# Performance work log

Hardware: AMD Instinct MI355X
Metric: run time of the kernel (lower is better)

The kernel has to match this reference:

```python
import jax, jax.numpy as jnp
import numpy as np

HIDDEN = 4096
NUM_HEADS = 32
HEAD_DIM = HIDDEN // NUM_HEADS  # 128, used only as softmax scale
CACHE_LEN = 100
BATCH = 8192


def setup_inputs() -> dict:
    key = jax.random.key(0)
    ks = jax.random.split(key, 7)
    return {
        "x": jax.random.normal(ks[0], (BATCH, HIDDEN), dtype=jnp.float32),
        "q_w": jax.random.normal(ks[1], (HIDDEN, HIDDEN), dtype=jnp.float32) * (1.0 / np.sqrt(HIDDEN)),
        "q_b": jax.random.normal(ks[2], (HIDDEN,), dtype=jnp.float32) * 0.01,
        "k_cache": jax.random.normal(ks[3], (CACHE_LEN, HIDDEN), dtype=jnp.float32),
        "v_cache": jax.random.normal(ks[4], (CACHE_LEN, HIDDEN), dtype=jnp.float32),
        "out_w": jax.random.normal(ks[5], (HIDDEN, HIDDEN), dtype=jnp.float32) * (1.0 / np.sqrt(HIDDEN)),
        "out_b": jax.random.normal(ks[6], (HIDDEN,), dtype=jnp.float32) * 0.01,
    }


def reference(x, q_w, q_b, k_cache, v_cache, out_w, out_b):
    # q_proj: torch Linear -> x @ W^T + b
    q = x @ q_w.T + q_b                                   # [N, H]
    # concat one zero row onto each cache (kv_len = CACHE_LEN + 1)
    k = jnp.concatenate([k_cache, jnp.zeros_like(k_cache[:1])], axis=0)  # [L+1, H]
    v = jnp.concatenate([v_cache, jnp.zeros_like(v_cache[:1])], axis=0)  # [L+1, H]
    scale = 1.0 / np.sqrt(HEAD_DIM).astype(np.float32)
    scores = (q @ k.T) * scale                            # [N, L+1]
    weights = jax.nn.softmax(scores, axis=-1)
    attn = weights @ v                                    # [N, H]
    return attn @ out_w.T + out_b                         # [N, H]
```

## Files before the change

kernel.cpp:

```cpp
#include <hip/hip_runtime.h>
#include <cstdio>

typedef __attribute__((ext_vector_type(8))) short short8;
typedef __attribute__((ext_vector_type(4))) float f32x4;


__device__ __forceinline__ unsigned short bf16r(float f) {
  union { float f; unsigned int u; } x; x.f = f;
  unsigned int r = x.u + 0x7fffu + ((x.u >> 16) & 1u);
  return (unsigned short)(r >> 16);
}

__device__ __forceinline__ float bf16f(unsigned short h) {
  union { unsigned int u; float f; } x; x.u = ((unsigned int)h) << 16;
  return x.f;
}

__device__ __forceinline__ void gload_lds16(const void* g, void* l) {
  __builtin_amdgcn_global_load_lds((const __attribute__((address_space(1))) void*)g,
                                   (__attribute__((address_space(3))) void*)l,
                                   16, 0, 0);
}

__device__ __forceinline__ short8 pack_bf16(float4 f0, float4 f1) {
  short8 h;
  h[0] = (short)bf16r(f0.x); h[1] = (short)bf16r(f0.y);
  h[2] = (short)bf16r(f0.z); h[3] = (short)bf16r(f0.w);
  h[4] = (short)bf16r(f1.x); h[5] = (short)bf16r(f1.y);
  h[6] = (short)bf16r(f1.z); h[7] = (short)bf16r(f1.w);
  return h;
}


__global__ void build_pad128(const float* __restrict__ src, unsigned short* __restrict__ dst) {
  int idx = blockIdx.x * blockDim.x + threadIdx.x;
  if (idx >= 128 * 4096) return;
  int row = idx >> 12;
  float v = (row < 100) ? src[idx] : 0.f;
  dst[idx] = bf16r(v);
}

__global__ void kq_bias(const float* __restrict__ kc, const float* __restrict__ qb,
                        float* __restrict__ sbias) {
  int l = blockIdx.x;
  int lane = threadIdx.x;
  float s = 0.f;
  if (l < 100) {
    for (int i = lane * 4; i < 4096; i += 256) {
      float4 k = *reinterpret_cast<const float4*>(kc + (size_t)l * 4096 + i);
      float4 q = *reinterpret_cast<const float4*>(qb + i);
      s += k.x * q.x + k.y * q.y + k.z * q.z + k.w * q.w;
    }
  }
  #pragma unroll
  for (int off = 1; off < 64; off <<= 1) s += __shfl_xor(s, off);
  if (lane == 0) sbias[l] = s;
}


__global__ __launch_bounds__(256)
void kq_fused(const unsigned short* __restrict__ Kp,
              const float* __restrict__ Qw,
              float* __restrict__ Cpart,
              int H, int jchunk) {
  __shared__ unsigned short Ak[128][32];
  __shared__ float Ts[32][129];

  const int tid = threadIdx.x, wave = tid >> 6, lane = tid & 63;
  const int wm = wave >> 1, wn = wave & 1;
  const int j0 = blockIdx.x * jchunk;
  const int i0 = blockIdx.y * 128;

  const int sr = wave * 16 + (lane >> 2);
  const int sc = (lane & 3) << 3;
  const unsigned short* Kp0 = Kp + (size_t)sr * H + j0 + sc;
  const unsigned short* Kp1 = Kp + (size_t)(64 + sr) * H + j0 + sc;
  unsigned short* AD0 = &Ak[wave * 16][0];
  unsigned short* AD1 = &Ak[64 + wave * 16][0];

  const int tj = tid >> 3;
  const int tc = (tid & 7) * 16;
  const float* Qp = Qw + (size_t)(j0 + tj) * H + i0 + tc;

  const int fr = lane & 15;
  const int kq = lane >> 4;

  f32x4 acc[4][4] = {};

  for (int jj = 0; jj < jchunk; jj += 32) {
    gload_lds16(Kp0 + jj, AD0);
    gload_lds16(Kp1 + jj, AD1);
    {
      const float* q = Qp + (size_t)jj * H;
      float4 v0 = *reinterpret_cast<const float4*>(q);
      float4 v1 = *reinterpret_cast<const float4*>(q + 4);
      float4 v2 = *reinterpret_cast<const float4*>(q + 8);
      float4 v3 = *reinterpret_cast<const float4*>(q + 12);
      Ts[tj][tc + 0]  = v0.x; Ts[tj][tc + 1]  = v0.y; Ts[tj][tc + 2]  = v0.z; Ts[tj][tc + 3]  = v0.w;
      Ts[tj][tc + 4]  = v1.x; Ts[tj][tc + 5]  = v1.y; Ts[tj][tc + 6]  = v1.z; Ts[tj][tc + 7]  = v1.w;
      Ts[tj][tc + 8]  = v2.x; Ts[tj][tc + 9]  = v2.y; Ts[tj][tc + 10] = v2.z; Ts[tj][tc + 11] = v2.w;
      Ts[tj][tc + 12] = v3.x; Ts[tj][tc + 13] = v3.y; Ts[tj][tc + 14] = v3.z; Ts[tj][tc + 15] = v3.w;
    }
    __syncthreads();

    short8 av[4];
    #pragma unroll
    for (int mi = 0; mi < 4; ++mi)
      av[mi] = *reinterpret_cast<const short8*>(&Ak[wm * 64 + mi * 16 + fr][kq * 8]);

    short8 bhi[4], blo[4];
    #pragma unroll
    for (int ni = 0; ni < 4; ++ni) {
      const int ic = wn * 64 + ni * 16 + fr;
      #pragma unroll
      for (int s = 0; s < 8; ++s) {
        float f = Ts[kq * 8 + s][ic];
        unsigned short h = bf16r(f);
        bhi[ni][s] = (short)h;
        blo[ni][s] = (short)bf16r(f - bf16f(h));
      }
    }

    #pragma unroll
    for (int mi = 0; mi < 4; ++mi)
      #pragma unroll
      for (int ni = 0; ni < 4; ++ni) {
        acc[mi][ni] = __builtin_amdgcn_mfma_f32_16x16x32_bf16(av[mi], bhi[ni], acc[mi][ni], 0, 0, 0);
        acc[mi][ni] = __builtin_amdgcn_mfma_f32_16x16x32_bf16(av[mi], blo[ni], acc[mi][ni], 0, 0, 0);
      }
    __syncthreads();
  }

  float* Cp = Cpart + (size_t)blockIdx.x * 128 * H;
  const int orow = (lane >> 4) * 4;
  const int ocol = lane & 15;
  #pragma unroll
  for (int mi = 0; mi < 4; ++mi) {
    #pragma unroll
    for (int ni = 0; ni < 4; ++ni) {
      size_t r0 = (size_t)wm * 64 + mi * 16 + orow;
      size_t c  = (size_t)i0 + wn * 64 + ni * 16 + ocol;
      #pragma unroll
      for (int j = 0; j < 4; ++j)
        Cp[(r0 + j) * (size_t)H + c] = acc[mi][ni][j];
    }
  }
}


template<int NB>
__global__ __launch_bounds__(256, 1)
void gemm_sv(const float* __restrict__ A, const unsigned short* __restrict__ B,
             float* __restrict__ Cpart, int M, int Kstride, int kchunk) {
  constexpr int FOLD = NB / 128;
  __shared__ float          As[2][128][32];
  __shared__ unsigned short Bs[2][NB][32];

  const int tid = threadIdx.x, wave = tid >> 6, lane = tid & 63;
  const int wm = wave >> 1, wn = wave & 1;
  const int ks = blockIdx.x, mblk = blockIdx.y;
  const size_t rowA0 = (size_t)mblk * 128;
  const int k0 = ks * kchunk;
  const int nsteps = kchunk >> 5;

  const int ar = lane >> 3;
  const int as_g = (lane & 7) ^ ar;
  const int br = lane >> 2;
  const int bs_g = (lane & 3) ^ (br & 3);

#define STAGE_SV(kt, BUF) do { \
    const int _kc = k0 + (kt) * 32; \
    _Pragma("unroll") \
    for (int j = 0; j < 4; ++j) \
      gload_lds16(A + (rowA0 + wave * 32 + j * 8 + ar) * (size_t)Kstride + _kc + as_g * 4, \
                  &As[BUF][wave * 32 + j * 8][0]); \
    _Pragma("unroll") \
    for (int j = 0; j < NB / 64; ++j) \
      gload_lds16(B + (size_t)(wave * (NB / 4) + j * 16 + br) * Kstride + _kc + bs_g * 8, \
                  &Bs[BUF][wave * (NB / 4) + j * 16][0]); \
  } while (0)

#define WAIT_STAGE do { \
    if (NB == 256) asm volatile("s_waitcnt vmcnt(8)" ::: "memory"); \
    else           asm volatile("s_waitcnt vmcnt(6)" ::: "memory"); \
  } while (0)

  const int fr = lane & 15, kq = lane >> 4;
  f32x4 acc[4][4] = {};

  STAGE_SV(0, 0);
  STAGE_SV(1, 1);
  WAIT_STAGE;
  asm volatile("" ::: "memory");
  __builtin_amdgcn_s_barrier();
  asm volatile("" ::: "memory");

  for (int k = 0; k < nsteps; ++k) {
    const int c = k & 1;

    short8 av[4], bv[4][FOLD];
    #pragma unroll
    for (int mi = 0; mi < 4; ++mi) {
      const float* rp = &As[c][wm * 64 + mi * 16 + fr][0];
      float4 f0 = *reinterpret_cast<const float4*>(rp + (((2 * kq)     ^ (fr & 7)) * 4));
      float4 f1 = *reinterpret_cast<const float4*>(rp + (((2 * kq + 1) ^ (fr & 7)) * 4));
      av[mi] = pack_bf16(f0, f1);
    }
    #pragma unroll
    for (int ni = 0; ni < 4; ++ni)
      #pragma unroll
      for (int p = 0; p < FOLD; ++p) {
        int rb = p * 128 + wn * 64 + ni * 16 + fr;
        bv[ni][p] = *reinterpret_cast<const short8*>(&Bs[c][rb][0] + ((kq ^ (fr & 3)) * 8));
      }

    asm volatile("s_waitcnt lgkmcnt(0)" ::: "memory");
    __builtin_amdgcn_s_barrier();
    asm volatile("" ::: "memory");

    const int kt2 = (k + 2 < nsteps) ? k + 2 : nsteps - 1;
    STAGE_SV(kt2, c);
    asm volatile("" ::: "memory");

    __builtin_amdgcn_s_setprio(1);
    #pragma unroll
    for (int mi = 0; mi < 4; ++mi)
      #pragma unroll
      for (int ni = 0; ni < 4; ++ni)
        #pragma unroll
        for (int p = 0; p < FOLD; ++p)
          acc[mi][ni] = __builtin_amdgcn_mfma_f32_16x16x32_bf16(av[mi], bv[ni][p], acc[mi][ni], 0, 0, 0);
    __builtin_amdgcn_s_setprio(0);

    WAIT_STAGE;
    asm volatile("" ::: "memory");
    __builtin_amdgcn_s_barrier();
    asm volatile("" ::: "memory");
  }

#undef STAGE_SV
#undef WAIT_STAGE

  float* Cp = Cpart + (size_t)ks * M * 128;
  const int orow = (lane >> 4) * 4;
  const int ocol = lane & 15;
  #pragma unroll
  for (int mi = 0; mi < 4; ++mi) {
    #pragma unroll
    for (int ni = 0; ni < 4; ++ni) {
      size_t r0 = rowA0 + wm * 64 + mi * 16 + orow;
      size_t c  = (size_t)wn * 64 + ni * 16 + ocol;
      #pragma unroll
      for (int j = 0; j < 4; ++j)
        Cp[(r0 + j) * 128 + c] = acc[mi][ni][j];
    }
  }
}


__global__ void kq_reduce(const float* __restrict__ KQpart, unsigned short* __restrict__ KQ2) {
  int idx = blockIdx.x * blockDim.x + threadIdx.x;
  if (idx >= 128 * 4096) return;
  float s = 0.f;
  #pragma unroll
  for (int ks = 0; ks < 8; ++ks) s += KQpart[(size_t)ks * 128 * 4096 + idx];
  unsigned short hi = bf16r(s);
  unsigned short lo = bf16r(s - bf16f(hi));
  int l = idx >> 12, j = idx & 4095;
  KQ2[(size_t)l * 4096 + j]         = hi;
  KQ2[(size_t)(l + 128) * 4096 + j] = lo;
}


__global__ void softmax_fused2(const float* __restrict__ Spart, const float* __restrict__ sbias,
                               unsigned short* __restrict__ W2, int rows) {
  int wave = threadIdx.x >> 6;
  int lane = threadIdx.x & 63;
  int row = blockIdx.x * (blockDim.x >> 6) + wave;
  if (row >= rows) return;
  const float scale = 0.088388347648318447f;
  float sx = 0.f, sy = 0.f;
  #pragma unroll
  for (int ks = 0; ks < 8; ++ks) {
    float2 p = reinterpret_cast<const float2*>(Spart + ((size_t)ks * rows + row) * 128)[lane];
    sx += p.x; sy += p.y;
  }
  float2 bb = reinterpret_cast<const float2*>(sbias)[lane];
  sx += bb.x; sy += bb.y;
  int c0 = lane * 2, c1 = c0 + 1;
  float s0 = (c0 <= 100) ? sx * scale : -1e30f;
  float s1 = (c1 <= 100) ? sy * scale : -1e30f;
  float m = fmaxf(s0, s1);
  #pragma unroll
  for (int off = 1; off < 64; off <<= 1) m = fmaxf(m, __shfl_xor(m, off));
  float e0 = (c0 <= 100) ? __expf(s0 - m) : 0.f;
  float e1 = (c1 <= 100) ? __expf(s1 - m) : 0.f;
  float sum = e0 + e1;
  #pragma unroll
  for (int off = 1; off < 64; off <<= 1) sum += __shfl_xor(sum, off);
  float inv = 1.f / sum;
  ushort2 o;
  o.x = bf16r(e0 * inv);
  o.y = bf16r(e1 * inv);
  reinterpret_cast<ushort2*>(W2 + (size_t)row * 256)[lane] = o;
  reinterpret_cast<ushort2*>(W2 + (size_t)row * 256 + 128)[lane] = o;
}


__global__ void vo_reduce(const float* __restrict__ VOpart, unsigned short* __restrict__ VOT2) {
  int idx = blockIdx.x * blockDim.x + threadIdx.x;
  if (idx >= 4096 * 128) return;
  float s = 0.f;
  #pragma unroll
  for (int ks = 0; ks < 16; ++ks) s += VOpart[(size_t)ks * 4096 * 128 + idx];
  unsigned short hi = bf16r(s);
  unsigned short lo = bf16r(s - bf16f(hi));
  int o = idx >> 7, l = idx & 127;
  VOT2[(size_t)o * 256 + l]       = hi;
  VOT2[(size_t)o * 256 + 128 + l] = lo;
}


__global__ __launch_bounds__(256)
void gemm_final(const unsigned short* __restrict__ A,
                const unsigned short* __restrict__ B,
                const float* __restrict__ bias,
                float* __restrict__ Cout,
                int M, int N, int K) {
  __shared__ unsigned short As[128][40];
  __shared__ unsigned short Bs[128][40];

  const int tid = threadIdx.x, wave = tid >> 6, lane = tid & 63;
  const int wm = wave >> 1, wn = wave & 1;
  const size_t rowA0 = (size_t)blockIdx.y * 128;
  const size_t colB0 = (size_t)blockIdx.x * 128;

  f32x4 acc[4][4] = {};

  const int srow  = tid >> 1;
  const int shalf = (tid & 1) * 16;

  const unsigned short* Ap = A + (rowA0 + srow) * (size_t)K + shalf;
  const unsigned short* Bp = B + (colB0 + srow) * (size_t)K + shalf;

  const int fr = lane & 15;
  const int fk = (lane >> 4) << 3;

  for (int k0 = 0; k0 < K; k0 += 32) {
    short8 a0 = *reinterpret_cast<const short8*>(Ap + k0);
    short8 a1 = *reinterpret_cast<const short8*>(Ap + k0 + 8);
    short8 b0 = *reinterpret_cast<const short8*>(Bp + k0);
    short8 b1 = *reinterpret_cast<const short8*>(Bp + k0 + 8);
    *reinterpret_cast<short8*>(&As[srow][shalf])     = a0;
    *reinterpret_cast<short8*>(&As[srow][shalf + 8]) = a1;
    *reinterpret_cast<short8*>(&Bs[srow][shalf])     = b0;
    *reinterpret_cast<short8*>(&Bs[srow][shalf + 8]) = b1;
    __syncthreads();

    short8 av[4], bv[4];
    #pragma unroll
    for (int mi = 0; mi < 4; ++mi)
      av[mi] = *reinterpret_cast<const short8*>(&As[wm * 64 + mi * 16 + fr][fk]);
    #pragma unroll
    for (int ni = 0; ni < 4; ++ni)
      bv[ni] = *reinterpret_cast<const short8*>(&Bs[wn * 64 + ni * 16 + fr][fk]);
    #pragma unroll
    for (int mi = 0; mi < 4; ++mi)
      #pragma unroll
      for (int ni = 0; ni < 4; ++ni)
        acc[mi][ni] = __builtin_amdgcn_mfma_f32_16x16x32_bf16(av[mi], bv[ni], acc[mi][ni], 0, 0, 0);
    __syncthreads();
  }

  const int orow = (lane >> 4) * 4;
  const int ocol = lane & 15;
  #pragma unroll
  for (int mi = 0; mi < 4; ++mi) {
    #pragma unroll
    for (int ni = 0; ni < 4; ++ni) {
      size_t r0 = rowA0 + wm * 64 + mi * 16 + orow;
      size_t c  = colB0 + wn * 64 + ni * 16 + ocol;
      float bv_ = bias[c];
      #pragma unroll
      for (int j = 0; j < 4; ++j)
        Cout[(r0 + j) * (size_t)N + c] = acc[mi][ni][j] + bv_;
    }
  }
}


extern "C" void kernel_launch(void* const* d_in, const int* in_sizes, int n_in,
                              void* d_out, int out_size, void* d_ws, size_t ws_size,
                              hipStream_t stream) {
  const float* x       = (const float*)d_in[0];
  const float* q_w     = (const float*)d_in[1];
  const float* q_b     = (const float*)d_in[2];
  const float* k_cache = (const float*)d_in[3];
  const float* v_cache = (const float*)d_in[4];
  const float* out_w   = (const float*)d_in[5];
  const float* out_b   = (const float*)d_in[6];
  float* out = (float*)d_out;

  const int M = 8192, H = 4096;

  char* ws = (char*)d_ws;
  size_t off = 0;
  auto alloc = [&](size_t bytes) { void* p = ws + off; off += (bytes + 255) & ~(size_t)255; return p; };
  unsigned short* kpad   = (unsigned short*)alloc((size_t)128 * H * 2);
  unsigned short* vpad   = (unsigned short*)alloc((size_t)128 * H * 2);
  float*          sbias  = (float*)alloc(128 * 4);
  unsigned short* KQ2    = (unsigned short*)alloc((size_t)256 * H * 2);
  unsigned short* W2     = (unsigned short*)alloc((size_t)M * 256 * 2);
  unsigned short* VOT2   = (unsigned short*)alloc((size_t)H * 256 * 2);
  float*          scratch= (float*)alloc((size_t)36 << 20);
  if (ws_size < off) { fprintf(stderr, "ws too small: need %zu have %zu\n", off, ws_size); return; }

  build_pad128<<<2048, 256, 0, stream>>>(k_cache, kpad);
  build_pad128<<<2048, 256, 0, stream>>>(v_cache, vpad);
  kq_bias<<<128, 64, 0, stream>>>(k_cache, q_b, sbias);

  kq_fused<<<dim3(8, 32), 256, 0, stream>>>(kpad, q_w, scratch, H, 512);
  kq_reduce<<<2048, 256, 0, stream>>>(scratch, KQ2);

  gemm_sv<256><<<dim3(8, 64), 256, 0, stream>>>(x, KQ2, scratch, M, H, 512);

  softmax_fused2<<<M / 4, 256, 0, stream>>>(scratch, sbias, W2, M);

  gemm_sv<128><<<dim3(16, 32), 256, 0, stream>>>(out_w, vpad, scratch, H, H, 256);
  vo_reduce<<<2048, 256, 0, stream>>>(scratch, VOT2);

  gemm_final<<<dim3(32, 64), 256, 0, stream>>>(W2, VOT2, out_b, out, M, H, 256);
}
```

Before: 188.4 us.

## Merge independent small kernels into horizontally fused launches to cut launch count

Result: faster. 162.0 us (median of 3 runs) (-14.0%).

```diff
diff --git a/kernel.cpp b/kernel.cpp
--- a/kernel.cpp
+++ b/kernel.cpp
@@ -32,44 +32,49 @@
 }
 
 
-__global__ void build_pad128(const float* __restrict__ src, unsigned short* __restrict__ dst) {
-  int idx = blockIdx.x * blockDim.x + threadIdx.x;
-  if (idx >= 128 * 4096) return;
-  int row = idx >> 12;
-  float v = (row < 100) ? src[idx] : 0.f;
-  dst[idx] = bf16r(v);
-}
-
-__global__ void kq_bias(const float* __restrict__ kc, const float* __restrict__ qb,
-                        float* __restrict__ sbias) {
-  int l = blockIdx.x;
-  int lane = threadIdx.x;
-  float s = 0.f;
-  if (l < 100) {
-    for (int i = lane * 4; i < 4096; i += 256) {
-      float4 k = *reinterpret_cast<const float4*>(kc + (size_t)l * 4096 + i);
-      float4 q = *reinterpret_cast<const float4*>(qb + i);
-      s += k.x * q.x + k.y * q.y + k.z * q.z + k.w * q.w;
-    }
-  }
-  #pragma unroll
-  for (int off = 1; off < 64; off <<= 1) s += __shfl_xor(s, off);
-  if (lane == 0) sbias[l] = s;
-}
-
-
-__global__ __launch_bounds__(256)
-void kq_fused(const unsigned short* __restrict__ Kp,
-              const float* __restrict__ Qw,
-              float* __restrict__ Cpart,
-              int H, int jchunk) {
-  __shared__ unsigned short Ak[128][32];
-  __shared__ float Ts[32][129];
+__global__ void prep(const float* __restrict__ kc, const float* __restrict__ vc,
+                     const float* __restrict__ qb,
+                     unsigned short* __restrict__ kpad, unsigned short* __restrict__ vpad,
+                     float* __restrict__ sbias) {
+  const int b = blockIdx.x, tid = threadIdx.x;
+  if (b < 4096) {
+    const bool isK = b < 2048;
+    const int bb = isK ? b : b - 2048;
+    int idx = bb * 256 + tid;
+    int row = idx >> 12;
+    const float* src = isK ? kc : vc;
+    float v = (row < 100) ? src[idx] : 0.f;
+    (isK ? kpad : vpad)[idx] = bf16r(v);
+  } else {
+    const int wave = tid >> 6, lane = tid & 63;
+    const int l = (b - 4096) * 4 + wave;
+    float s = 0.f;
+    if (l < 100) {
+      for (int i = lane * 4; i < 4096; i += 256) {
+        float4 k = *reinterpret_cast<const float4*>(kc + (size_t)l * 4096 + i);
+        float4 q = *reinterpret_cast<const float4*>(qb + i);
+        s += k.x * q.x + k.y * q.y + k.z * q.z + k.w * q.w;
+      }
+    }
+    #pragma unroll
+    for (int off = 1; off < 64; off <<= 1) s += __shfl_xor(s, off);
+    if (lane == 0) sbias[l] = s;
+  }
+}
+
+
+__device__ __forceinline__ void kq_fused_body(const unsigned short* __restrict__ Kp,
+                                              const float* __restrict__ Qw,
+                                              float* __restrict__ Cpart,
+                                              int H, int jchunk, int js, int itile,
+                                              char* smem) {
+  unsigned short (*Ak)[32] = (unsigned short (*)[32])smem;
+  float (*Ts)[129] = (float (*)[129])(smem + 8192);
 
   const int tid = threadIdx.x, wave = tid >> 6, lane = tid & 63;
   const int wm = wave >> 1, wn = wave & 1;
-  const int j0 = blockIdx.x * jchunk;
-  const int i0 = blockIdx.y * 128;
+  const int j0 = js * jchunk;
+  const int i0 = itile * 128;
 
   const int sr = wave * 16 + (lane >> 2);
   const int sc = (lane & 3) << 3;
@@ -131,7 +136,7 @@
     __syncthreads();
   }
 
-  float* Cp = Cpart + (size_t)blockIdx.x * 128 * H;
+  float* Cp = Cpart + (size_t)js * 128 * H;
   const int orow = (lane >> 4) * 4;
   const int ocol = lane & 15;
   #pragma unroll
@@ -149,16 +154,17 @@
 
 
 template<int NB>
-__global__ __launch_bounds__(256, 1)
-void gemm_sv(const float* __restrict__ A, const unsigned short* __restrict__ B,
-             float* __restrict__ Cpart, int M, int Kstride, int kchunk) {
+__device__ __forceinline__ void gemm_sv_body(const float* __restrict__ A,
+                                             const unsigned short* __restrict__ B,
+                                             float* __restrict__ Cpart,
+                                             int M, int Kstride, int kchunk,
+                                             int ks, int mblk, char* smem) {
   constexpr int FOLD = NB / 128;
-  __shared__ float          As[2][128][32];
-  __shared__ unsigned short Bs[2][NB][32];
+  float (*As)[128][32] = (float (*)[128][32])smem;
+  unsigned short (*Bs)[NB][32] = (unsigned short (*)[NB][32])(smem + 32768);
 
   const int tid = threadIdx.x, wave = tid >> 6, lane = tid & 63;
   const int wm = wave >> 1, wn = wave & 1;
-  const int ks = blockIdx.x, mblk = blockIdx.y;
   const size_t rowA0 = (size_t)mblk * 128;
   const int k0 = ks * kchunk;
   const int nsteps = kchunk >> 5;
@@ -258,17 +264,54 @@
 }
 
 
-__global__ void kq_reduce(const float* __restrict__ KQpart, unsigned short* __restrict__ KQ2) {
-  int idx = blockIdx.x * blockDim.x + threadIdx.x;
-  if (idx >= 128 * 4096) return;
-  float s = 0.f;
-  #pragma unroll
-  for (int ks = 0; ks < 8; ++ks) s += KQpart[(size_t)ks * 128 * 4096 + idx];
-  unsigned short hi = bf16r(s);
-  unsigned short lo = bf16r(s - bf16f(hi));
-  int l = idx >> 12, j = idx & 4095;
-  KQ2[(size_t)l * 4096 + j]         = hi;
-  KQ2[(size_t)(l + 128) * 4096 + j] = lo;
+__global__ __launch_bounds__(256, 1)
+void fused_kqvo(const unsigned short* __restrict__ kpad, const float* __restrict__ qw,
+                float* __restrict__ KQpart,
+                const float* __restrict__ outw, const unsigned short* __restrict__ vpad,
+                float* __restrict__ VOpart, int H) {
+  __shared__ __align__(16) char smem[49152];
+  const int b = blockIdx.x;
+  if (b < 256) {
+    kq_fused_body(kpad, qw, KQpart, H, 512, b & 7, b >> 3, smem);
+  } else {
+    const int b2 = b - 256;
+    gemm_sv_body<128>(outw, vpad, VOpart, H, H, 256, b2 & 15, b2 >> 4, smem);
+  }
+}
+
+
+__global__ __launch_bounds__(256, 1)
+void gemm_s(const float* __restrict__ A, const unsigned short* __restrict__ B,
+            float* __restrict__ Cpart, int M, int Kstride, int kchunk) {
+  __shared__ __align__(16) char smem[65536];
+  gemm_sv_body<256>(A, B, Cpart, M, Kstride, kchunk, blockIdx.x, blockIdx.y, smem);
+}
+
+
+__global__ void reduces(const float* __restrict__ KQpart, unsigned short* __restrict__ KQ2,
+                        const float* __restrict__ VOpart, unsigned short* __restrict__ VOT2) {
+  const int b = blockIdx.x;
+  if (b < 2048) {
+    int idx = b * 256 + threadIdx.x;
+    float s = 0.f;
+    #pragma unroll
+    for (int ks = 0; ks < 8; ++ks) s += KQpart[(size_t)ks * 128 * 4096 + idx];
+    unsigned short hi = bf16r(s);
+    unsigned short lo = bf16r(s - bf16f(hi));
+    int l = idx >> 12, j = idx & 4095;
+    KQ2[(size_t)l * 4096 + j]         = hi;
+    KQ2[(size_t)(l + 128) * 4096 + j] = lo;
+  } else {
+    int idx = (b - 2048) * 256 + threadIdx.x;
+    float s = 0.f;
+    #pragma unroll
+    for (int ks = 0; ks < 16; ++ks) s += VOpart[(size_t)ks * 4096 * 128 + idx];
+    unsigned short hi = bf16r(s);
+    unsigned short lo = bf16r(s - bf16f(hi));
+    int o = idx >> 7, l = idx & 127;
+    VOT2[(size_t)o * 256 + l]       = hi;
+    VOT2[(size_t)o * 256 + 128 + l] = lo;
+  }
 }
 
 
@@ -304,20 +347,6 @@
   o.y = bf16r(e1 * inv);
   reinterpret_cast<ushort2*>(W2 + (size_t)row * 256)[lane] = o;
   reinterpret_cast<ushort2*>(W2 + (size_t)row * 256 + 128)[lane] = o;
-}
-
-
-__global__ void vo_reduce(const float* __restrict__ VOpart, unsigned short* __restrict__ VOT2) {
-  int idx = blockIdx.x * blockDim.x + threadIdx.x;
-  if (idx >= 4096 * 128) return;
-  float s = 0.f;
-  #pragma unroll
-  for (int ks = 0; ks < 16; ++ks) s += VOpart[(size_t)ks * 4096 * 128 + idx];
-  unsigned short hi = bf16r(s);
-  unsigned short lo = bf16r(s - bf16f(hi));
-  int o = idx >> 7, l = idx & 127;
-  VOT2[(size_t)o * 256 + l]       = hi;
-  VOT2[(size_t)o * 256 + 128 + l] = lo;
 }
 
 
@@ -412,22 +441,20 @@
   unsigned short* KQ2    = (unsigned short*)alloc((size_t)256 * H * 2);
   unsigned short* W2     = (unsigned short*)alloc((size_t)M * 256 * 2);
   unsigned short* VOT2   = (unsigned short*)alloc((size_t)H * 256 * 2);
-  float*          scratch= (float*)alloc((size_t)36 << 20);
+  float*          KQpart = (float*)alloc((size_t)8 * 128 * H * 4);
+  float*          VOpart = (float*)alloc((size_t)16 * H * 128 * 4);
+  float*          Spart  = VOpart;
   if (ws_size < off) { fprintf(stderr, "ws too small: need %zu have %zu\n", off, ws_size); return; }
 
-  build_pad128<<<2048, 256, 0, stream>>>(k_cache, kpad);
-  build_pad128<<<2048, 256, 0, stream>>>(v_cache, vpad);
-  kq_bias<<<128, 64, 0, stream>>>(k_cache, q_b, sbias);
-
-  kq_fused<<<dim3(8, 32), 256, 0, stream>>>(kpad, q_w, scratch, H, 512);
-  kq_reduce<<<2048, 256, 0, stream>>>(scratch, KQ2);
-
-  gemm_sv<256><<<dim3(8, 64), 256, 0, stream>>>(x, KQ2, scratch, M, H, 512);
-
-  softmax_fused2<<<M / 4, 256, 0, stream>>>(scratch, sbias, W2, M);
-
-  gemm_sv<128><<<dim3(16, 32), 256, 0, stream>>>(out_w, vpad, scratch, H, H, 256);
-  vo_reduce<<<2048, 256, 0, stream>>>(scratch, VOT2);
+  prep<<<4128, 256, 0, stream>>>(k_cache, v_cache, q_b, kpad, vpad, sbias);
+
+  fused_kqvo<<<768, 256, 0, stream>>>(kpad, q_w, KQpart, out_w, vpad, VOpart, H);
+
+  reduces<<<4096, 256, 0, stream>>>(KQpart, KQ2, VOpart, VOT2);
+
+  gemm_s<<<dim3(8, 64), 256, 0, stream>>>(x, KQ2, Spart, M, H, 512);
+
+  softmax_fused2<<<M / 4, 256, 0, stream>>>(Spart, sbias, W2, M);
 
   gemm_final<<<dim3(32, 64), 256, 0, stream>>>(W2, VOT2, out_b, out, M, H, 256);
 }
```
